# Optimization experiments

Hardware: AMD Instinct MI355X
Metric: run time of the kernel (lower is better)

## Reference

```python
import jax, jax.numpy as jnp
import numpy as np

TEMPERATURE = 0.07


def setup_inputs() -> dict:
    key = jax.random.key(0)
    k1, k2 = jax.random.split(key)
    B, D = 8192, 256
    embeddings = jax.random.normal(k1, (B, D), dtype=jnp.float32)
    ids = jax.random.randint(k2, (B,), 0, 1024, dtype=jnp.int64 if jax.config.jax_enable_x64 else jnp.int32)
    return {"embeddings": embeddings, "ids": ids}


def reference(embeddings, ids):
    B = embeddings.shape[0]
    # L2-normalize rows (F.normalize with p=2, dim=1)
    emb = embeddings / jnp.maximum(jnp.linalg.norm(embeddings, axis=1, keepdims=True), 1e-12)
    sim = (emb @ emb.T) / TEMPERATURE                      # [B, B]
    eye = jnp.eye(B, dtype=bool)
    sim = jnp.where(eye, -jnp.inf, sim)
    exp_sim = jnp.exp(sim)                                  # diag -> 0
    pos_mask = (ids[:, None] == ids[None, :]) & ~eye        # [B, B]
    pos_sum = jnp.sum(jnp.where(pos_mask, exp_sim, 0.0), axis=1)  # [B]
    all_sum = jnp.sum(exp_sim, axis=1)                      # [B]
    valid = pos_mask.any(axis=1)
    per_row = -jnp.log(pos_sum / all_sum)
    loss = jnp.sum(jnp.where(valid, per_row, 0.0))
    n_valid = jnp.sum(valid.astype(jnp.float32))
    return loss / jnp.maximum(n_valid, 1.0)
```

## Files before the change

### kernel.cpp

```cpp
#include <hip/hip_runtime.h>
#include <hip/hip_bf16.h>

#define B_SZ 8192
#define D_SZ 256
#define INV_T 14.285714285714286f

typedef __attribute__((ext_vector_type(4))) float f32x4;
typedef __attribute__((ext_vector_type(8))) short s16x8;

__device__ __forceinline__ void async_copy16(const void* g, void* l) {
    __builtin_amdgcn_global_load_lds(
        (const __attribute__((address_space(1))) unsigned int*)g,
        (__attribute__((address_space(3))) unsigned int*)l,
        16, 0, 0);
}

__global__ __launch_bounds__(256) void norm_kernel(const float* __restrict__ emb,
                                                   ushort* __restrict__ nbf,
                                                   float* __restrict__ sums) {
    if (blockIdx.x < 64) sums[blockIdx.x * 256 + threadIdx.x] = 0.0f;

    int wave = threadIdx.x >> 6, lane = threadIdx.x & 63;
    int row  = blockIdx.x * 4 + wave;
    const float4 v = ((const float4*)(emb + (size_t)row * D_SZ))[lane];
    float ss = v.x * v.x + v.y * v.y + v.z * v.z + v.w * v.w;
    #pragma unroll
    for (int m = 1; m < 64; m <<= 1) ss += __shfl_xor(ss, m, 64);
    float s = 1.0f / fmaxf(sqrtf(ss), 1e-12f);
    __hip_bfloat16 b0 = __float2bfloat16(v.x * s);
    __hip_bfloat16 b1 = __float2bfloat16(v.y * s);
    __hip_bfloat16 b2 = __float2bfloat16(v.z * s);
    __hip_bfloat16 b3 = __float2bfloat16(v.w * s);
    ushort4 o;
    o.x = *(ushort*)&b0; o.y = *(ushort*)&b1; o.z = *(ushort*)&b2; o.w = *(ushort*)&b3;
    ((ushort4*)(nbf + (size_t)row * D_SZ))[lane] = o;
}

__global__ __launch_bounds__(256) void sim_kernel(const ushort* __restrict__ N,
                                                  const int* __restrict__ ids,
                                                  float* __restrict__ all_sum,
                                                  float* __restrict__ pos_sum) {
    __shared__ ushort sA[128 * 64];
    __shared__ ushort sB[128 * 64];
    __shared__ int   sIdR[128], sIdC[128];

    const int t    = threadIdx.x;
    const int wave = t >> 6, lane = t & 63;
    const int wy   = wave >> 1, wx = wave & 1;

    int tb = blockIdx.x;
    int bj = (int)((sqrtf(8.0f * tb + 1.0f) - 1.0f) * 0.5f);
    while ((bj + 1) * (bj + 2) / 2 <= tb) ++bj;
    while (bj * (bj + 1) / 2 > tb) --bj;
    const int bi   = tb - bj * (bj + 1) / 2;
    const int i0   = bi * 128;
    const int j0   = bj * 128;
    const bool diag = (bi == bj);

    if (t < 128) sIdR[t] = ids[i0 + t];
    else         sIdC[t - 128] = ids[j0 + (t - 128)];

    f32x4 acc[4][4];
    #pragma unroll
    for (int mi = 0; mi < 4; ++mi)
        #pragma unroll
        for (int ni = 0; ni < 4; ++ni)
            acc[mi][ni] = (f32x4){0.f, 0.f, 0.f, 0.f};

    const int r  = lane >> 3;
    const int c8 = (lane & 7) * 8;

    for (int kk = 0; kk < 4; ++kk) {
        const int k0 = kk * 64;
        const ushort* gA = N + (size_t)(i0 + wave * 32) * D_SZ + k0;
        const ushort* gB = N + (size_t)(j0 + wave * 32) * D_SZ + k0;
        #pragma unroll
        for (int q = 0; q < 4; ++q) {
            async_copy16(gA + (size_t)(q * 8 + r) * D_SZ + c8, &sA[(wave * 32 + q * 8) * 64]);
            async_copy16(gB + (size_t)(q * 8 + r) * D_SZ + c8, &sB[(wave * 32 + q * 8) * 64]);
        }
        __syncthreads();

        #pragma unroll
        for (int ks = 0; ks < 2; ++ks) {
            const int ko = ks * 32 + (lane >> 4) * 8;
            s16x8 af[4], bf[4];
            #pragma unroll
            for (int mi = 0; mi < 4; ++mi)
                af[mi] = *(const s16x8*)&sA[(wy * 64 + mi * 16 + (lane & 15)) * 64 + ko];
            #pragma unroll
            for (int ni = 0; ni < 4; ++ni)
                bf[ni] = *(const s16x8*)&sB[(wx * 64 + ni * 16 + (lane & 15)) * 64 + ko];
            #pragma unroll
            for (int mi = 0; mi < 4; ++mi)
                #pragma unroll
                for (int ni = 0; ni < 4; ++ni)
                    acc[mi][ni] = __builtin_amdgcn_mfma_f32_16x16x32_bf16(
                        af[mi], bf[ni], acc[mi][ni], 0, 0, 0);
        }
        __syncthreads();
    }

    float* rowAllPart = (float*)sA;
    float* rowPosPart = (float*)sB;
    const int myc = lane & 15;

    float cAll[4] = {0.f, 0.f, 0.f, 0.f};
    float cPos[4] = {0.f, 0.f, 0.f, 0.f};

    #pragma unroll
    for (int mi = 0; mi < 4; ++mi) {
        float rAll[4] = {0.f, 0.f, 0.f, 0.f};
        float rPos[4] = {0.f, 0.f, 0.f, 0.f};
        const int rbase = wy * 64 + mi * 16 + (lane >> 4) * 4;
        #pragma unroll
        for (int ni = 0; ni < 4; ++ni) {
            const int cloc = wx * 64 + ni * 16 + myc;
            const int gj   = j0 + cloc;
            const int idc  = sIdC[cloc];
            #pragma unroll
            for (int rg = 0; rg < 4; ++rg) {
                const int lr = rbase + rg;
                float e = __expf(acc[mi][ni][rg] * INV_T);
                if (diag && (i0 + lr) == gj) e = 0.0f;
                rAll[rg] += e; cAll[ni] += e;
                if (sIdR[lr] == idc) { rPos[rg] += e; cPos[ni] += e; }
            }
        }
        #pragma unroll
        for (int rg = 0; rg < 4; ++rg) {
            rowAllPart[(rbase + rg) * 17 + myc] = rAll[rg];
            rowPosPart[(rbase + rg) * 17 + myc] = rPos[rg];
        }
    }

    if (!diag) {
        #pragma unroll
        for (int ni = 0; ni < 4; ++ni) {
            cAll[ni] += __shfl_xor(cAll[ni], 16, 64);
            cAll[ni] += __shfl_xor(cAll[ni], 32, 64);
            cPos[ni] += __shfl_xor(cPos[ni], 16, 64);
            cPos[ni] += __shfl_xor(cPos[ni], 32, 64);
        }
        if (lane < 16) {
            #pragma unroll
            for (int ni = 0; ni < 4; ++ni) {
                const int gc = j0 + wx * 64 + ni * 16 + lane;
                atomicAdd(&all_sum[gc], cAll[ni]);
                atomicAdd(&pos_sum[gc], cPos[ni]);
            }
        }
    }

    __syncthreads();
    {
        const int row = t & 127;
        const float* src = (t >= 128) ? rowPosPart : rowAllPart;
        float s = 0.0f;
        #pragma unroll
        for (int k = 0; k < 16; ++k) s += src[row * 17 + k];
        float* dst = (t >= 128) ? pos_sum : all_sum;
        atomicAdd(&dst[i0 + row], s);
    }
}

__global__ __launch_bounds__(256) void loss_kernel(const float* __restrict__ all_sum,
                                                   const float* __restrict__ pos_sum,
                                                   float* __restrict__ out) {
    float loss = 0.0f, cnt = 0.0f;
    for (int i = threadIdx.x; i < B_SZ; i += 256) {
        float p = pos_sum[i], a = all_sum[i];
        if (p > 0.0f) { loss += logf(a) - logf(p); cnt += 1.0f; }
    }
    #pragma unroll
    for (int m = 1; m < 64; m <<= 1) {
        loss += __shfl_xor(loss, m, 64);
        cnt  += __shfl_xor(cnt, m, 64);
    }
    __shared__ float sl[4], sc[4];
    int wave = threadIdx.x >> 6, lane = threadIdx.x & 63;
    if (lane == 0) { sl[wave] = loss; sc[wave] = cnt; }
    __syncthreads();
    if (threadIdx.x == 0) {
        float L = sl[0] + sl[1] + sl[2] + sl[3];
        float C = sc[0] + sc[1] + sc[2] + sc[3];
        out[0] = L / fmaxf(C, 1.0f);
    }
}

extern "C" void kernel_launch(void* const* d_in, const int* in_sizes, int n_in,
                              void* d_out, int out_size, void* d_ws, size_t ws_size,
                              hipStream_t stream) {
    const float* emb = (const float*)d_in[0];
    const int*   ids = (const int*)d_in[1];
    float*       out = (float*)d_out;

    float*  all_sum = (float*)d_ws;
    float*  pos_sum = all_sum + B_SZ;
    ushort* nbf     = (ushort*)((char*)d_ws + 65536);

    norm_kernel<<<B_SZ / 4, 256, 0, stream>>>(emb, nbf, all_sum);
    const int ntiles = (B_SZ / 128) * (B_SZ / 128 + 1) / 2;
    sim_kernel<<<ntiles, 256, 0, stream>>>(nbf, ids, all_sum, pos_sum);
    loss_kernel<<<1, 256, 0, stream>>>(all_sum, pos_sum, out);
}
```

Before: 130.8 us.

## Load MFMA fragments directly from global, fold temperature into normalization

The sim kernel no longer stages A/B tiles through LDS with async copies and per-step barriers. Each wave now loads its bf16 fragments straight from global memory, with the K loop fully unrolled, and the kernel requests higher occupancy through launch bounds. The 1/T scale is folded into the normalization as sqrt(1/T) per vector, which removes a multiply from the exp epilogue. The row-partial LDS buffer is widened so the two column-half waves no longer overwrite each other's partials, which also fixes a race. The trade-off is relying on cache hits for the fragment data that the waves share, instead of an explicit LDS reuse path.

```diff
diff --git a/kernel.cpp b/kernel.cpp
--- a/kernel.cpp
+++ b/kernel.cpp
@@ -3,17 +3,10 @@
 
 #define B_SZ 8192
 #define D_SZ 256
-#define INV_T 14.285714285714286f
+#define SQRT_INV_T 3.7796447300922722f
 
 typedef __attribute__((ext_vector_type(4))) float f32x4;
 typedef __attribute__((ext_vector_type(8))) short s16x8;
-
-__device__ __forceinline__ void async_copy16(const void* g, void* l) {
-    __builtin_amdgcn_global_load_lds(
-        (const __attribute__((address_space(1))) unsigned int*)g,
-        (__attribute__((address_space(3))) unsigned int*)l,
-        16, 0, 0);
-}
 
 __global__ __launch_bounds__(256) void norm_kernel(const float* __restrict__ emb,
                                                    ushort* __restrict__ nbf,
@@ -26,7 +19,7 @@
     float ss = v.x * v.x + v.y * v.y + v.z * v.z + v.w * v.w;
     #pragma unroll
     for (int m = 1; m < 64; m <<= 1) ss += __shfl_xor(ss, m, 64);
-    float s = 1.0f / fmaxf(sqrtf(ss), 1e-12f);
+    float s = SQRT_INV_T / fmaxf(sqrtf(ss), 1e-12f);
     __hip_bfloat16 b0 = __float2bfloat16(v.x * s);
     __hip_bfloat16 b1 = __float2bfloat16(v.y * s);
     __hip_bfloat16 b2 = __float2bfloat16(v.z * s);
@@ -36,12 +29,11 @@
     ((ushort4*)(nbf + (size_t)row * D_SZ))[lane] = o;
 }
 
-__global__ __launch_bounds__(256) void sim_kernel(const ushort* __restrict__ N,
-                                                  const int* __restrict__ ids,
-                                                  float* __restrict__ all_sum,
-                                                  float* __restrict__ pos_sum) {
-    __shared__ ushort sA[128 * 64];
-    __shared__ ushort sB[128 * 64];
+__global__ __launch_bounds__(256, 3) void sim_kernel(const ushort* __restrict__ N,
+                                                     const int* __restrict__ ids,
+                                                     float* __restrict__ all_sum,
+                                                     float* __restrict__ pos_sum) {
+    __shared__ float sPart[2 * 128 * 33];
     __shared__ int   sIdR[128], sIdC[128];
 
     const int t    = threadIdx.x;
@@ -67,42 +59,30 @@
         for (int ni = 0; ni < 4; ++ni)
             acc[mi][ni] = (f32x4){0.f, 0.f, 0.f, 0.f};
 
-    const int r  = lane >> 3;
-    const int c8 = (lane & 7) * 8;
+    const ushort* baseA = N + (size_t)(i0 + wy * 64 + (lane & 15)) * D_SZ + (lane >> 4) * 8;
+    const ushort* baseB = N + (size_t)(j0 + wx * 64 + (lane & 15)) * D_SZ + (lane >> 4) * 8;
 
-    for (int kk = 0; kk < 4; ++kk) {
-        const int k0 = kk * 64;
-        const ushort* gA = N + (size_t)(i0 + wave * 32) * D_SZ + k0;
-        const ushort* gB = N + (size_t)(j0 + wave * 32) * D_SZ + k0;
+    #pragma unroll
+    for (int kb = 0; kb < 8; ++kb) {
+        s16x8 af[4], bf[4];
         #pragma unroll
-        for (int q = 0; q < 4; ++q) {
-            async_copy16(gA + (size_t)(q * 8 + r) * D_SZ + c8, &sA[(wave * 32 + q * 8) * 64]);
-            async_copy16(gB + (size_t)(q * 8 + r) * D_SZ + c8, &sB[(wave * 32 + q * 8) * 64]);
-        }
-        __syncthreads();
-
+        for (int mi = 0; mi < 4; ++mi)
+            af[mi] = *(const s16x8*)(baseA + mi * 16 * D_SZ + kb * 32);
         #pragma unroll
-        for (int ks = 0; ks < 2; ++ks) {
-            const int ko = ks * 32 + (lane >> 4) * 8;
-            s16x8 af[4], bf[4];
-            #pragma unroll
-            for (int mi = 0; mi < 4; ++mi)
-                af[mi] = *(const s16x8*)&sA[(wy * 64 + mi * 16 + (lane & 15)) * 64 + ko];
+        for (int ni = 0; ni < 4; ++ni)
+            bf[ni] = *(const s16x8*)(baseB + ni * 16 * D_SZ + kb * 32);
+        #pragma unroll
+        for (int mi = 0; mi < 4; ++mi)
             #pragma unroll
             for (int ni = 0; ni < 4; ++ni)
-                bf[ni] = *(const s16x8*)&sB[(wx * 64 + ni * 16 + (lane & 15)) * 64 + ko];
-            #pragma unroll
-            for (int mi = 0; mi < 4; ++mi)
-                #pragma unroll
-                for (int ni = 0; ni < 4; ++ni)
-                    acc[mi][ni] = __builtin_amdgcn_mfma_f32_16x16x32_bf16(
-                        af[mi], bf[ni], acc[mi][ni], 0, 0, 0);
-        }
-        __syncthreads();
+                acc[mi][ni] = __builtin_amdgcn_mfma_f32_16x16x32_bf16(
+                    af[mi], bf[ni], acc[mi][ni], 0, 0, 0);
     }
 
-    float* rowAllPart = (float*)sA;
-    float* rowPosPart = (float*)sB;
+    __syncthreads();
+
+    float* rowAllPart = sPart;
+    float* rowPosPart = sPart + 128 * 33;
     const int myc = lane & 15;
 
     float cAll[4] = {0.f, 0.f, 0.f, 0.f};
@@ -116,21 +96,20 @@
         #pragma unroll
         for (int ni = 0; ni < 4; ++ni) {
             const int cloc = wx * 64 + ni * 16 + myc;
-            const int gj   = j0 + cloc;
             const int idc  = sIdC[cloc];
             #pragma unroll
             for (int rg = 0; rg < 4; ++rg) {
                 const int lr = rbase + rg;
-                float e = __expf(acc[mi][ni][rg] * INV_T);
-                if (diag && (i0 + lr) == gj) e = 0.0f;
+                float e = __expf(acc[mi][ni][rg]);
+                if (diag && lr == cloc) e = 0.0f;
                 rAll[rg] += e; cAll[ni] += e;
                 if (sIdR[lr] == idc) { rPos[rg] += e; cPos[ni] += e; }
             }
         }
         #pragma unroll
         for (int rg = 0; rg < 4; ++rg) {
-            rowAllPart[(rbase + rg) * 17 + myc] = rAll[rg];
-            rowPosPart[(rbase + rg) * 17 + myc] = rPos[rg];
+            rowAllPart[(rbase + rg) * 33 + wx * 16 + myc] = rAll[rg];
+            rowPosPart[(rbase + rg) * 33 + wx * 16 + myc] = rPos[rg];
         }
     }
 
@@ -158,7 +137,7 @@
         const float* src = (t >= 128) ? rowPosPart : rowAllPart;
         float s = 0.0f;
         #pragma unroll
-        for (int k = 0; k < 16; ++k) s += src[row * 17 + k];
+        for (int k = 0; k < 32; ++k) s += src[row * 33 + k];
         float* dst = (t >= 128) ? pos_sum : all_sum;
         atomicAdd(&dst[i0 + row], s);
     }
```

Result: slower. 155.4 us (+18.8%).
